# Kernel optimization log

Measured on AMD Instinct MI355X. Metric: run time of the kernel, lower is better.

The kernel has to match this reference:

```python
import jax, jax.numpy as jnp
import numpy as np

EMBED = 1024
HEADS = 16
HD = EMBED // HEADS          # 64
M = 32                       # num_features
R = 2                        # num_quadrature_nodes
EPS = 1e-06
C_CONST = 2.0 + EPS
CHUNK = 512


def setup_inputs() -> dict:
    key = jax.random.key(0)
    ks = jax.random.split(key, 4)
    B, T = 2, 2048
    x = jax.random.normal(ks[0], (B, T, EMBED), jnp.float32)
    Wqkv = jax.random.normal(ks[1], (EMBED, 3 * EMBED), jnp.float32) * 0.02
    bqkv = jnp.zeros((3 * EMBED,), jnp.float32)
    Wout = jax.random.normal(ks[2], (EMBED, EMBED), jnp.float32) * 0.02
    bout = jnp.zeros((EMBED,), jnp.float32)
    omega = jax.random.normal(ks[3], (R, HEADS, HD, M), jnp.float32)
    # Gauss-Laguerre quadrature buffers (deterministic)
    nodes, weights = np.polynomial.laguerre.laggauss(R)
    quad_nodes = jnp.asarray(nodes / C_CONST, jnp.float32)
    quad_weights = jnp.asarray(weights * (C_CONST / 4.0), jnp.float32)
    return {"x": x, "Wqkv": Wqkv, "bqkv": bqkv, "Wout": Wout, "bout": bout,
            "omega": omega, "quad_nodes": quad_nodes, "quad_weights": quad_weights}


def _features(x, omega, quad_nodes, quad_weights):
    # x: (B,H,T,D) -> Laplace PRF features (B,H,T,R*M)
    B, H, T, D = x.shape
    xn = x / jnp.maximum(jnp.linalg.norm(x, axis=-1, keepdims=True), 1e-12)
    proj = jnp.einsum('bhtd,rhdm->rbhtm', xn, omega)
    s = quad_nodes[:, None, None, None, None]
    sqrt_2s = jnp.sqrt(2.0 * jnp.maximum(s, 0.0))
    arg = jnp.clip(proj * sqrt_2s - s, -20.0, 20.0)
    feat = jnp.exp(arg) / np.sqrt(M).astype(np.float32)
    feat = feat * jnp.sqrt(jnp.maximum(quad_weights, 0.0))[:, None, None, None, None]
    return jnp.transpose(feat, (1, 2, 3, 0, 4)).reshape(B, H, T, R * M)


def reference(x, Wqkv, bqkv, Wout, bout, omega, quad_nodes, quad_weights):
    B, T, C = x.shape
    qkv = x @ Wqkv + bqkv
    q, k, v = jnp.split(qkv, 3, axis=-1)
    resh = lambda t: t.reshape(B, T, HEADS, HD).transpose(0, 2, 1, 3)  # (B,H,T,D)
    q, k, v = resh(q), resh(k), resh(v)
    qf = _features(q, omega, quad_nodes, quad_weights)   # (B,H,T,F)
    kf = _features(k, omega, quad_nodes, quad_weights)
    Fd = R * M
    nc = T // CHUNK
    # -> (nc, B, H, chunk, .)
    to_chunks = lambda t, last: t.reshape(B, HEADS, nc, CHUNK, last).transpose(2, 0, 1, 3, 4)
    qc = to_chunks(qf, Fd)
    kc = to_chunks(kf, Fd)
    vc = to_chunks(v, HD)

    def step(carry, inp):
        kv_state, k_state = carry                        # (B,H,F,D), (B,H,F)
        q_ch, k_ch, v_ch = inp
        kv_prod = jnp.einsum('bhtf,bhtd->bhtfd', k_ch, v_ch)
        kv_cur = jnp.cumsum(kv_prod, axis=2) + kv_state[:, :, None]
        k_cur = jnp.cumsum(k_ch, axis=2) + k_state[:, :, None]
        ctx = jnp.einsum('bhtf,bhtfd->bhtd', q_ch, kv_cur)
        den = jnp.maximum(jnp.einsum('bhtf,bhtf->bht', q_ch, k_cur), 1e-06)
        out_ch = ctx / den[..., None]
        return (kv_cur[:, :, -1], k_cur[:, :, -1]), out_ch

    init = (jnp.zeros((B, HEADS, Fd, HD), jnp.float32),
            jnp.zeros((B, HEADS, Fd), jnp.float32))
    _, outs = jax.lax.scan(step, init, (qc, kc, vc))     # (nc,B,H,chunk,D)
    out = outs.transpose(1, 2, 0, 3, 4).reshape(B, HEADS, T, HD)
    out = out.transpose(0, 2, 1, 3).reshape(B, T, C)
    return out @ Wout + bout
```

## Files before the change

kernel.cpp:

```cpp
#include <hip/hip_runtime.h>
#include <cstddef>
#include <cstdint>

#define B_ 2
#define T_ 2048
#define EMBED_ 1024
#define HEADS_ 16
#define HD_ 64
#define M_ 32
#define R_ 2
#define FD_ 64
#define LCH 64
#define NCH (T_ / LCH)
#define BH_ (B_ * HEADS_)

typedef unsigned short u16;
using bf16x8 = __attribute__((ext_vector_type(8))) short;
using f16x8 = __attribute__((ext_vector_type(8))) _Float16;
using f32x4 = __attribute__((ext_vector_type(4))) float;

__device__ __forceinline__ u16 f2bf(float f) {
  uint32_t u = __float_as_uint(f);
  u += 0x7FFF + ((u >> 16) & 1);
  return (u16)(u >> 16);
}
__device__ __forceinline__ float bf2f(u16 h) {
  return __uint_as_float(((uint32_t)h) << 16);
}
__device__ __forceinline__ u16 f2h(float f) {
  _Float16 h = (_Float16)f;
  return *(u16*)&h;
}
__device__ __forceinline__ _Float16 f2hh(float f) { return (_Float16)f; }

__device__ __forceinline__ void gload_lds16(const void* g, void* l) {
  __builtin_amdgcn_global_load_lds(
      (const __attribute__((address_space(1))) unsigned int*)g,
      (__attribute__((address_space(3))) unsigned int*)l, 16, 0, 0);
}

__device__ __forceinline__ int swz_off(int R, int s) {
  return (R >> 1) * 64 + (((((R & 1) << 2) | s) ^ ((R >> 1) & 7)) * 8);
}

__global__ __launch_bounds__(256) void gemm_f16_k(
    const u16* __restrict__ A, const u16* __restrict__ Bt,
    const float* __restrict__ bias, float* __restrict__ C, int K, int ldc)
{
  __shared__ u16 As[2][128 * 32];
  __shared__ u16 Bs[2][128 * 32];
  const int tid = threadIdx.x;
  const int row0 = blockIdx.y * 128, col0 = blockIdx.x * 128;
  const int lane = tid & 63;
  const int w = tid >> 6;
  const int wr = tid >> 7, wc = (tid >> 6) & 1;
  f32x4 acc[4][4];
#pragma unroll
  for (int m = 0; m < 4; ++m)
#pragma unroll
    for (int n = 0; n < 4; ++n)
#pragma unroll
      for (int r = 0; r < 4; ++r) acc[m][n][r] = 0.f;

  const int u_ = (lane & 7) ^ (lane >> 3);
  const int srow = w * 16 + 2 * (lane >> 3) + (u_ >> 2);
  const int skp = (u_ & 3) * 8;
  const u16* Agp = A + (size_t)(row0 + srow) * K + skp;
  const u16* Bgp = Bt + (size_t)(col0 + srow) * K + skp;
  const int wb = w * 512;

  const int fr = lane & 15;
  const int s_ = lane >> 4;
  int aoff[4], boff[4];
#pragma unroll
  for (int m = 0; m < 4; ++m) aoff[m] = swz_off(wr * 64 + m * 16 + fr, s_);
#pragma unroll
  for (int n = 0; n < 4; ++n) boff[n] = swz_off(wc * 64 + n * 16 + fr, s_);

  const int nt = K >> 5;
  gload_lds16(Agp, &As[0][wb]);
  gload_lds16(Agp + (size_t)64 * K, &As[0][wb + 2048]);
  gload_lds16(Bgp, &Bs[0][wb]);
  gload_lds16(Bgp + (size_t)64 * K, &Bs[0][wb + 2048]);
  __syncthreads();

  for (int t = 0; t < nt; ++t) {
    const int cur = t & 1;
    if (t + 1 < nt) {
      const int k0 = (t + 1) * 32;
      gload_lds16(Agp + k0, &As[cur ^ 1][wb]);
      gload_lds16(Agp + k0 + (size_t)64 * K, &As[cur ^ 1][wb + 2048]);
      gload_lds16(Bgp + k0, &Bs[cur ^ 1][wb]);
      gload_lds16(Bgp + k0 + (size_t)64 * K, &Bs[cur ^ 1][wb + 2048]);
    }
    f16x8 a[4], b[4];
#pragma unroll
    for (int m = 0; m < 4; ++m) a[m] = *(const f16x8*)&As[cur][aoff[m]];
#pragma unroll
    for (int n = 0; n < 4; ++n) b[n] = *(const f16x8*)&Bs[cur][boff[n]];
#pragma unroll
    for (int m = 0; m < 4; ++m)
#pragma unroll
      for (int n = 0; n < 4; ++n)
        acc[m][n] = __builtin_amdgcn_mfma_f32_16x16x32_f16(a[m], b[n],
                                                           acc[m][n], 0, 0, 0);
    __syncthreads();
  }
  const int fg = lane >> 4;
#pragma unroll
  for (int m = 0; m < 4; ++m) {
#pragma unroll
    for (int n = 0; n < 4; ++n) {
      const int col = col0 + wc * 64 + n * 16 + fr;
      const float bv = bias[col];
#pragma unroll
      for (int r = 0; r < 4; ++r) {
        const int row = row0 + wr * 64 + m * 16 + fg * 4 + r;
        C[(size_t)row * ldc + col] = acc[m][n][r] + bv;
      }
    }
  }
}

__global__ __launch_bounds__(256) void gemm_f16_n64_k(
    const u16* __restrict__ A, const u16* __restrict__ Bt,
    const float* __restrict__ bias, float* __restrict__ C, int K, int ldc)
{
  __shared__ u16 As[2][128 * 32];
  __shared__ u16 Bs[2][64 * 32];
  const int tid = threadIdx.x;
  const int row0 = blockIdx.y * 128, col0 = blockIdx.x * 64;
  const int lane = tid & 63;
  const int w = tid >> 6;
  f32x4 acc[2][4];
#pragma unroll
  for (int m = 0; m < 2; ++m)
#pragma unroll
    for (int n = 0; n < 4; ++n)
#pragma unroll
      for (int r = 0; r < 4; ++r) acc[m][n][r] = 0.f;

  const int u_ = (lane & 7) ^ (lane >> 3);
  const int srow = w * 16 + 2 * (lane >> 3) + (u_ >> 2);
  const int skp = (u_ & 3) * 8;
  const u16* Agp = A + (size_t)(row0 + srow) * K + skp;
  const u16* Bgp = Bt + (size_t)(col0 + srow) * K + skp;
  const int wb = w * 512;

  const int fr = lane & 15;
  const int s_ = lane >> 4;
  int aoff[2], boff[4];
#pragma unroll
  for (int m = 0; m < 2; ++m) aoff[m] = swz_off(w * 32 + m * 16 + fr, s_);
#pragma unroll
  for (int n = 0; n < 4; ++n) boff[n] = swz_off(n * 16 + fr, s_);

  const int nt = K >> 5;
  gload_lds16(Agp, &As[0][wb]);
  gload_lds16(Agp + (size_t)64 * K, &As[0][wb + 2048]);
  gload_lds16(Bgp, &Bs[0][wb]);
  __syncthreads();

  for (int t = 0; t < nt; ++t) {
    const int cur = t & 1;
    if (t + 1 < nt) {
      const int k0 = (t + 1) * 32;
      gload_lds16(Agp + k0, &As[cur ^ 1][wb]);
      gload_lds16(Agp + k0 + (size_t)64 * K, &As[cur ^ 1][wb + 2048]);
      gload_lds16(Bgp + k0, &Bs[cur ^ 1][wb]);
    }
    f16x8 a[2], b[4];
#pragma unroll
    for (int m = 0; m < 2; ++m) a[m] = *(const f16x8*)&As[cur][aoff[m]];
#pragma unroll
    for (int n = 0; n < 4; ++n) b[n] = *(const f16x8*)&Bs[cur][boff[n]];
#pragma unroll
    for (int m = 0; m < 2; ++m)
#pragma unroll
      for (int n = 0; n < 4; ++n)
        acc[m][n] = __builtin_amdgcn_mfma_f32_16x16x32_f16(a[m], b[n],
                                                           acc[m][n], 0, 0, 0);
    __syncthreads();
  }
  const int fg = lane >> 4;
#pragma unroll
  for (int m = 0; m < 2; ++m) {
#pragma unroll
    for (int n = 0; n < 4; ++n) {
      const int col = col0 + n * 16 + fr;
      const float bv = bias[col];
#pragma unroll
      for (int r = 0; r < 4; ++r) {
        const int row = row0 + w * 32 + m * 16 + fg * 4 + r;
        C[(size_t)row * ldc + col] = acc[m][n][r] + bv;
      }
    }
  }
}

__global__ __launch_bounds__(256) void cvt_x_f16_k(const float* __restrict__ X,
                                                   u16* __restrict__ Y, int n8)
{
  const int idx = blockIdx.x * 256 + threadIdx.x;
  if (idx >= n8) return;
  float4 a = *(const float4*)&X[(size_t)idx * 8];
  float4 b = *(const float4*)&X[(size_t)idx * 8 + 4];
  ushort4 o0, o1;
  o0.x = f2h(a.x); o0.y = f2h(a.y); o0.z = f2h(a.z); o0.w = f2h(a.w);
  o1.x = f2h(b.x); o1.y = f2h(b.y); o1.z = f2h(b.z); o1.w = f2h(b.w);
  *(ushort4*)&Y[(size_t)idx * 8] = o0;
  *(ushort4*)&Y[(size_t)idx * 8 + 4] = o1;
}

__global__ __launch_bounds__(256) void cvt_w_f16t_k(const float* __restrict__ W,
                                                    u16* __restrict__ Wt, int N)
{
  __shared__ float tile[32][33];
  const int n0 = blockIdx.x * 32, k0 = blockIdx.y * 32;
  const int tx = threadIdx.x & 31, ty = threadIdx.x >> 5;
#pragma unroll
  for (int i = 0; i < 4; ++i)
    tile[ty + i * 8][tx] = W[(size_t)(k0 + ty + i * 8) * N + n0 + tx];
  __syncthreads();
#pragma unroll
  for (int i = 0; i < 4; ++i) {
    const int n = ty + i * 8;
    Wt[(size_t)(n0 + n) * 1024 + k0 + tx] = f2h(tile[tx][n]);
  }
}

__global__ __launch_bounds__(256) void gemm_bias_k(
    const float* __restrict__ A, const float* __restrict__ Bm,
    const float* __restrict__ bias, float* __restrict__ C,
    int Mdim, int Ndim, int Kdim, int lda, int ldb, int ldc)
{
  __shared__ float Asm[16][128];
  __shared__ float Bsm[16][128];
  const int tid = threadIdx.x;
  const int row0 = blockIdx.y * 128;
  const int col0 = blockIdx.x * 128;
  const int ty = tid >> 4, tx = tid & 15;
  float acc[8][8];
#pragma unroll
  for (int i = 0; i < 8; ++i)
#pragma unroll
    for (int j = 0; j < 8; ++j) acc[i][j] = 0.f;

  for (int k0 = 0; k0 < Kdim; k0 += 16) {
#pragma unroll
    for (int l = 0; l < 2; ++l) {
      int f = tid * 2 + l;
      int ar = f >> 2, aq = f & 3;
      float4 av = *reinterpret_cast<const float4*>(
          &A[(size_t)(row0 + ar) * lda + k0 + aq * 4]);
      Asm[aq * 4 + 0][ar] = av.x;
      Asm[aq * 4 + 1][ar] = av.y;
      Asm[aq * 4 + 2][ar] = av.z;
      Asm[aq * 4 + 3][ar] = av.w;
      int br = f >> 5, bc = f & 31;
      *reinterpret_cast<float4*>(&Bsm[br][bc * 4]) =
          *reinterpret_cast<const float4*>(
              &Bm[(size_t)(k0 + br) * ldb + col0 + bc * 4]);
    }
    __syncthreads();
#pragma unroll
    for (int kk = 0; kk < 16; ++kk) {
      float a[8], b[8];
      *reinterpret_cast<float4*>(&a[0]) =
          *reinterpret_cast<const float4*>(&Asm[kk][ty * 8]);
      *reinterpret_cast<float4*>(&a[4]) =
          *reinterpret_cast<const float4*>(&Asm[kk][ty * 8 + 4]);
      *reinterpret_cast<float4*>(&b[0]) =
          *reinterpret_cast<const float4*>(&Bsm[kk][tx * 8]);
      *reinterpret_cast<float4*>(&b[4]) =
          *reinterpret_cast<const float4*>(&Bsm[kk][tx * 8 + 4]);
#pragma unroll
      for (int i = 0; i < 8; ++i)
#pragma unroll
        for (int j = 0; j < 8; ++j) acc[i][j] += a[i] * b[j];
    }
    __syncthreads();
  }
#pragma unroll
  for (int i = 0; i < 8; ++i) {
    int r = row0 + ty * 8 + i;
#pragma unroll
    for (int j = 0; j < 8; j += 4) {
      int c = col0 + tx * 8 + j;
      float4 o;
      o.x = acc[i][j + 0] + bias[c + 0];
      o.y = acc[i][j + 1] + bias[c + 1];
      o.z = acc[i][j + 2] + bias[c + 2];
      o.w = acc[i][j + 3] + bias[c + 3];
      *reinterpret_cast<float4*>(&C[(size_t)r * ldc + c]) = o;
    }
  }
}

__global__ __launch_bounds__(256) void features_mfma_k(
    const float* __restrict__ qkv, const float* __restrict__ omega,
    const float* __restrict__ qnodes, const float* __restrict__ qweights,
    float* __restrict__ qf, float* __restrict__ kf)
{
  __shared__ u16 Aext[64 * 200];
  __shared__ u16 Bext[64 * 200];
  __shared__ float rinv_s[64];
  const int tid = threadIdx.x;
  const int t0 = blockIdx.x * 64;
  const int h = blockIdx.y;
  const int b = blockIdx.z & 1;
  const int which = blockIdx.z >> 1;
  const int bh = b * HEADS_ + h;

  {
    const int row = tid >> 2;
    const int seg = (tid & 3) * 16;
    const float* xsrc = &qkv[((size_t)(b * T_ + t0 + row)) * 3072 +
                             which * 1024 + h * 64 + seg];
    float xv[16];
#pragma unroll
    for (int q = 0; q < 4; ++q)
      *(float4*)&xv[q * 4] = *(const float4*)&xsrc[q * 4];
    float ss = 0.f;
#pragma unroll
    for (int j = 0; j < 16; ++j) ss += xv[j] * xv[j];
    ss += __shfl_xor(ss, 1, 64);
    ss += __shfl_xor(ss, 2, 64);
    if ((tid & 3) == 0) rinv_s[row] = 1.f / fmaxf(sqrtf(ss), 1e-12f);
    ushort4 hv[4], lv[4];
    u16* hp = (u16*)hv; u16* lp = (u16*)lv;
#pragma unroll
    for (int j = 0; j < 16; ++j) {
      u16 hh = f2bf(xv[j]);
      hp[j] = hh;
      lp[j] = f2bf(xv[j] - bf2f(hh));
    }
    u16* arow = &Aext[row * 200 + seg];
#pragma unroll
    for (int q = 0; q < 4; ++q) {
      *(ushort4*)&arow[q * 4] = hv[q];
      *(ushort4*)&arow[64 + q * 4] = lv[q];
      *(ushort4*)&arow[128 + q * 4] = hv[q];
    }
  }
  {
    const int r_o = tid >> 7;
    const int dseg = (tid >> 5) & 3;
    const int m_o = tid & 31;
    const int n = r_o * 32 + m_o;
    const size_t obase =
        (((size_t)(r_o * HEADS_ + h)) * HD_ + dseg * 16) * M_ + m_o;
    ushort4 hv[4], lv[4];
    u16* hp = (u16*)hv; u16* lp = (u16*)lv;
#pragma unroll
    for (int i = 0; i < 16; ++i) {
      float v = omega[obase + (size_t)i * M_];
      u16 hh = f2bf(v);
      hp[i] = hh;
      lp[i] = f2bf(v - bf2f(hh));
    }
    u16* brow = &Bext[n * 200 + dseg * 16];
#pragma unroll
    for (int q = 0; q < 4; ++q) {
      *(ushort4*)&brow[q * 4] = hv[q];
      *(ushort4*)&brow[64 + q * 4] = hv[q];
      *(ushort4*)&brow[128 + q * 4] = lv[q];
    }
  }
  __syncthreads();

  const int lane = tid & 63;
  const int w = tid >> 6;
  const int fr = lane & 15, s_ = lane >> 4;
  f32x4 facc[4];
#pragma unroll
  for (int n = 0; n < 4; ++n)
#pragma unroll
    for (int r = 0; r < 4; ++r) facc[n][r] = 0.f;
  const u16* arow = &Aext[(w * 16 + fr) * 200 + s_ * 8];
#pragma unroll
  for (int kk = 0; kk < 6; ++kk) {
    bf16x8 av = *(const bf16x8*)&arow[kk * 32];
#pragma unroll
    for (int n = 0; n < 4; ++n) {
      bf16x8 bv = *(const bf16x8*)&Bext[(n * 16 + fr) * 200 + kk * 32 + s_ * 8];
      facc[n] = __builtin_amdgcn_mfma_f32_16x16x32_bf16(av, bv, facc[n], 0, 0, 0);
    }
  }

  const float s0 = qnodes[0], s1 = qnodes[1];
  const float sq0 = sqrtf(2.f * fmaxf(s0, 0.f));
  const float sq1 = sqrtf(2.f * fmaxf(s1, 0.f));
  const float sc0 = sqrtf(fmaxf(qweights[0], 0.f)) * 0.17677669529663687f;
  const float sc1 = sqrtf(fmaxf(qweights[1], 0.f)) * 0.17677669529663687f;
  float* __restrict__ dst = which ? kf : qf;
  const size_t base = ((size_t)bh * T_ + t0) * FD_;
  const int fg = lane >> 4;
#pragma unroll
  for (int n = 0; n < 4; ++n) {
    const int feat = n * 16 + fr;
    const int ridx = n >> 1;
    const float sq = ridx ? sq1 : sq0;
    const float so = ridx ? s1 : s0;
    const float sc = ridx ? sc1 : sc0;
#pragma unroll
    for (int j = 0; j < 4; ++j) {
      const int token = w * 16 + fg * 4 + j;
      const float pr = facc[n][j] * rinv_s[token];
      float arg = fminf(fmaxf(pr * sq - so, -20.f), 20.f);
      dst[base + (size_t)token * FD_ + feat] = expf(arg) * sc;
    }
  }
}

__global__ __launch_bounds__(256) void chunk_sums_k(
    const float* __restrict__ kf, const float* __restrict__ qkv,
    float* __restrict__ kvsum, float* __restrict__ ksum)
{
  const int blk = blockIdx.x;
  const int c = blk % NCH;
  const int bh = blk / NCH;
  const int b = bh / HEADS_, h = bh % HEADS_;
  const int tid = threadIdx.x;
  const int d = tid & 63;
  const int fq = tid >> 6;
  __shared__ float kf_s[16][64];
  __shared__ float v_s[16][64];
  float acc[16];
#pragma unroll
  for (int i = 0; i < 16; ++i) acc[i] = 0.f;
  float ks = 0.f;
  for (int t0 = 0; t0 < LCH; t0 += 16) {
#pragma unroll
    for (int l = 0; l < 4; ++l) {
      int idx = tid + l * 256;
      int rr = idx >> 6, cc = idx & 63;
      int t = c * LCH + t0 + rr;
      kf_s[rr][cc] = kf[((size_t)bh * T_ + t) * FD_ + cc];
      v_s[rr][cc] =
          qkv[((size_t)(b * T_ + t)) * 3072 + 2 * EMBED_ + h * HD_ + cc];
    }
    __syncthreads();
#pragma unroll
    for (int tt = 0; tt < 16; ++tt) {
      float vv = v_s[tt][d];
      if (fq == 0) ks += kf_s[tt][d];
#pragma unroll
      for (int i = 0; i < 16; ++i) acc[i] += kf_s[tt][fq * 16 + i] * vv;
    }
    __syncthreads();
  }
#pragma unroll
  for (int i = 0; i < 16; ++i)
    kvsum[(size_t)blk * 4096 + (size_t)(fq * 16 + i) * 64 + d] = acc[i];
  if (fq == 0) ksum[(size_t)blk * 64 + d] = ks;
}

__global__ __launch_bounds__(256) void prefix2_k(float* __restrict__ kvsum,
                                                 float* __restrict__ ksum)
{
  const int bh = blockIdx.x >> 4;
  const int eb = blockIdx.x & 15;
  const int e = eb * 256 + threadIdx.x;
  float v[NCH];
  const size_t base = (size_t)bh * NCH * 4096 + e;
#pragma unroll
  for (int c = 0; c < NCH; ++c) v[c] = kvsum[base + (size_t)c * 4096];
  float run = 0.f;
#pragma unroll
  for (int c = 0; c < NCH; ++c) {
    kvsum[base + (size_t)c * 4096] = run;
    run += v[c];
  }
  if (eb == 0 && threadIdx.x < 64) {
    const size_t kb = (size_t)bh * NCH * 64 + threadIdx.x;
    float w[NCH];
#pragma unroll
    for (int c = 0; c < NCH; ++c) w[c] = ksum[kb + c * 64];
    float r2 = 0.f;
#pragma unroll
    for (int c = 0; c < NCH; ++c) {
      ksum[kb + c * 64] = r2;
      r2 += w[c];
    }
  }
}

__global__ __launch_bounds__(256) void chunk_attn4_k(
    const float* __restrict__ qf, const float* __restrict__ kf,
    const float* __restrict__ qkv_v, const float* __restrict__ kvsum,
    const float* __restrict__ ksum, u16* __restrict__ out_f16)
{
  constexpr float SCL = 1.f / 1024.f;
  constexpr float DEN_EPS = 1e-6f / 1024.f;
  __shared__ u16 qf_h[64 * 72];
  __shared__ u16 kf_h[64 * 72];
  __shared__ u16 st_h[64 * 72];
  __shared__ u16 vt_h[64 * 72];
  __shared__ u16 p_h[64 * 72];
  __shared__ float den_s[64];
  const int blk = blockIdx.x;
  const int c = blk & (NCH - 1);
  const int bh = blk / NCH;
  const int b = bh / HEADS_, h = bh % HEADS_;
  const int tid = threadIdx.x;

  {
    const int r = tid >> 2, q4 = (tid & 3) * 16;
    const size_t fbase = ((size_t)bh * T_ + c * LCH + r) * FD_ + q4;
    const size_t vbase =
        ((size_t)(b * T_ + c * LCH + r)) * 3072 + 2 * EMBED_ + h * HD_ + q4;
    const size_t sbase = (size_t)blk * 4096 + (size_t)r * 64 + q4;
    float qv[16], kv[16], sv[16], vv[16], ks[16];
#pragma unroll
    for (int j = 0; j < 16; j += 4) {
      *(float4*)&qv[j] = *(const float4*)&qf[fbase + j];
      *(float4*)&kv[j] = *(const float4*)&kf[fbase + j];
      *(float4*)&sv[j] = *(const float4*)&kvsum[sbase + j];
      *(float4*)&vv[j] = *(const float4*)&qkv_v[vbase + j];
      *(float4*)&ks[j] = *(const float4*)&ksum[(size_t)blk * 64 + q4 + j];
    }
    float dh = 0.f;
#pragma unroll
    for (int j = 0; j < 16; ++j) dh += qv[j] * ks[j];
    dh += __shfl_xor(dh, 1, 64);
    dh += __shfl_xor(dh, 2, 64);
    if ((tid & 3) == 0) den_s[r] = dh * SCL;
    ushort4 qo[4], ko[4];
    u16* qp = (u16*)qo; u16* kp = (u16*)ko;
#pragma unroll
    for (int j = 0; j < 16; ++j) { qp[j] = f2h(qv[j]); kp[j] = f2h(kv[j]); }
#pragma unroll
    for (int q = 0; q < 4; ++q) {
      *(ushort4*)&qf_h[r * 72 + q4 + q * 4] = qo[q];
      *(ushort4*)&kf_h[r * 72 + q4 + q * 4] = ko[q];
    }
#pragma unroll
    for (int j = 0; j < 16; ++j) {
      st_h[(q4 + j) * 72 + r] = f2h(sv[j] * SCL);
      vt_h[(q4 + j) * 72 + r] = f2h(vv[j]);
    }
  }
  __syncthreads();

  const int lane = tid & 63;
  const int w = tid >> 6;
  const int fr = lane & 15;
  const int s_ = lane >> 4;
  const int arow = (w * 16 + fr) * 72 + s_ * 8;
  const int trow = w * 16 + s_ * 4;

  const f16x8 a0 = *(const f16x8*)&qf_h[arow];
  const f16x8 a1 = *(const f16x8*)&qf_h[arow + 32];

  f32x4 sc[4];
#pragma unroll
  for (int n = 0; n < 4; ++n) {
#pragma unroll
    for (int r = 0; r < 4; ++r) sc[n][r] = 0.f;
    const f16x8 b0 = *(const f16x8*)&kf_h[(n * 16 + fr) * 72 + s_ * 8];
    const f16x8 b1 = *(const f16x8*)&kf_h[(n * 16 + fr) * 72 + 32 + s_ * 8];
    sc[n] = __builtin_amdgcn_mfma_f32_16x16x32_f16(a0, b0, sc[n], 0, 0, 0);
    sc[n] = __builtin_amdgcn_mfma_f32_16x16x32_f16(a1, b1, sc[n], 0, 0, 0);
  }
  f32x4 acc[4];
#pragma unroll
  for (int n = 0; n < 4; ++n) {
#pragma unroll
    for (int r = 0; r < 4; ++r) acc[n][r] = 0.f;
    const f16x8 b0 = *(const f16x8*)&st_h[(n * 16 + fr) * 72 + s_ * 8];
    const f16x8 b1 = *(const f16x8*)&st_h[(n * 16 + fr) * 72 + 32 + s_ * 8];
    acc[n] = __builtin_amdgcn_mfma_f32_16x16x32_f16(a0, b0, acc[n], 0, 0, 0);
    acc[n] = __builtin_amdgcn_mfma_f32_16x16x32_f16(a1, b1, acc[n], 0, 0, 0);
  }
  float den2[4] = {0.f, 0.f, 0.f, 0.f};
#pragma unroll
  for (int n = 0; n < 4; ++n) {
    const int scol = n * 16 + fr;
#pragma unroll
    for (int r = 0; r < 4; ++r) {
      const int t = trow + r;
      const float v = (scol <= t) ? sc[n][r] : 0.f;
      p_h[t * 72 + scol] = f2h(v * SCL);
      den2[r] += v;
    }
  }
#pragma unroll
  for (int r = 0; r < 4; ++r) {
    float d = den2[r];
    d += __shfl_xor(d, 1, 64);
    d += __shfl_xor(d, 2, 64);
    d += __shfl_xor(d, 4, 64);
    d += __shfl_xor(d, 8, 64);
    den2[r] = d;
  }
  if (fr == 0) {
#pragma unroll
    for (int r = 0; r < 4; ++r) den_s[trow + r] += den2[r] * SCL;
  }
  __syncthreads();

  const f16x8 p0 = *(const f16x8*)&p_h[arow];
  const f16x8 p1 = *(const f16x8*)&p_h[arow + 32];
#pragma unroll
  for (int n = 0; n < 4; ++n) {
    const f16x8 b0 = *(const f16x8*)&vt_h[(n * 16 + fr) * 72 + s_ * 8];
    const f16x8 b1 = *(const f16x8*)&vt_h[(n * 16 + fr) * 72 + 32 + s_ * 8];
    acc[n] = __builtin_amdgcn_mfma_f32_16x16x32_f16(p0, b0, acc[n], 0, 0, 0);
    acc[n] = __builtin_amdgcn_mfma_f32_16x16x32_f16(p1, b1, acc[n], 0, 0, 0);
  }

  float rden[4];
#pragma unroll
  for (int r = 0; r < 4; ++r)
    rden[r] = 1.f / fmaxf(den_s[trow + r], DEN_EPS);
#pragma unroll
  for (int n = 0; n < 4; ++n) {
    const int d = n * 16 + fr;
#pragma unroll
    for (int r = 0; r < 4; ++r) {
      const int t = trow + r;
      out_f16[((size_t)(b * T_ + c * LCH + t)) * 1024 + h * HD_ + d] =
          f2h(acc[n][r] * rden[r]);
    }
  }
}

__global__ __launch_bounds__(256) void chunk_attn3_k(
    const float* __restrict__ qf, const float* __restrict__ kf,
    const float* __restrict__ qkv_v, const float* __restrict__ kvsum,
    const float* __restrict__ ksum, float* __restrict__ out_f32, int lda)
{
  const int blk = blockIdx.x;
  const int c = blk & (NCH - 1);
  const int bh = blk / NCH;
  const int b = bh / HEADS_, h = bh % HEADS_;
  const int tid = threadIdx.x;
  __shared__ float kf_s[64][64];
  __shared__ float v_s[64][64];
  __shared__ float S_s[64][64];
  __shared__ float qf_s[64][64];
  {
    const int r = tid >> 2, q4 = (tid & 3) * 16;
    const size_t fbase = ((size_t)bh * T_ + c * LCH + r) * FD_ + q4;
    const size_t vbase =
        ((size_t)(b * T_ + c * LCH + r)) * 3072 + 2 * EMBED_ + h * HD_ + q4;
    const size_t sbase = (size_t)blk * 4096 + (size_t)r * 64 + q4;
#pragma unroll
    for (int j = 0; j < 16; j += 4) {
      *(float4*)&kf_s[r][q4 + j] = *(const float4*)&kf[fbase + j];
      *(float4*)&qf_s[r][q4 + j] = *(const float4*)&qf[fbase + j];
      *(float4*)&S_s[r][q4 + j] = *(const float4*)&kvsum[sbase + j];
      *(float4*)&v_s[r][q4 + j] = *(const float4*)&qkv_v[vbase + j];
    }
  }
  __syncthreads();
  const int l = tid & 63;
  const int t = (tid >> 6) * 16 + (l & 15);
  const int dq = l >> 4, d0 = dq * 16;

  float q_r[64];
#pragma unroll
  for (int j = 0; j < 64; j += 4)
    *(float4*)&q_r[j] = *(const float4*)&qf_s[t][j];

  float ctx[16];
#pragma unroll
  for (int j = 0; j < 16; ++j) ctx[j] = 0.f;
  float den = 0.f, den2 = 0.f;

#pragma unroll 4
  for (int f = 0; f < 64; ++f) {
    const float qv = q_r[f];
#pragma unroll
    for (int j = 0; j < 16; j += 4) {
      float4 s4 = *(const float4*)&S_s[f][d0 + j];
      ctx[j + 0] += qv * s4.x;
      ctx[j + 1] += qv * s4.y;
      ctx[j + 2] += qv * s4.z;
      ctx[j + 3] += qv * s4.w;
    }
  }
  {
    const float* svp = &ksum[(size_t)blk * 64 + d0];
#pragma unroll
    for (int j = 0; j < 16; ++j) den += q_r[d0 + j] * svp[j];
  }

  for (int s = 0; s < LCH; ++s) {
    float a = 0.f;
#pragma unroll
    for (int j = 0; j < 16; j += 4) {
      float4 k4 = *(const float4*)&kf_s[s][d0 + j];
      a += q_r[d0 + j] * k4.x + q_r[d0 + j + 1] * k4.y +
           q_r[d0 + j + 2] * k4.z + q_r[d0 + j + 3] * k4.w;
    }
    a += __shfl_xor(a, 16, 64);
    a += __shfl_xor(a, 32, 64);
    if (s <= t) {
      den2 += a;
#pragma unroll
      for (int j = 0; j < 16; j += 4) {
        float4 v4 = *(const float4*)&v_s[s][d0 + j];
        ctx[j + 0] += a * v4.x;
        ctx[j + 1] += a * v4.y;
        ctx[j + 2] += a * v4.z;
        ctx[j + 3] += a * v4.w;
      }
    }
  }
  den += __shfl_xor(den, 16, 64);
  den += __shfl_xor(den, 32, 64);
  const float rden = 1.f / fmaxf(den + den2, 1e-6f);
  float* op = &out_f32[((size_t)(b * T_ + c * LCH + t)) * lda + h * HD_ + d0];
#pragma unroll
  for (int j = 0; j < 16; j += 4) {
    float4 o;
    o.x = ctx[j + 0] * rden;
    o.y = ctx[j + 1] * rden;
    o.z = ctx[j + 2] * rden;
    o.w = ctx[j + 3] * rden;
    *(float4*)&op[j] = o;
  }
}

extern "C" void kernel_launch(void* const* d_in, const int* in_sizes, int n_in,
                              void* d_out, int out_size, void* d_ws,
                              size_t ws_size, hipStream_t stream)
{
  (void)in_sizes; (void)n_in; (void)out_size;
  const float* x = (const float*)d_in[0];
  const float* Wqkv = (const float*)d_in[1];
  const float* bqkv = (const float*)d_in[2];
  const float* Wout = (const float*)d_in[3];
  const float* bout = (const float*)d_in[4];
  const float* omega = (const float*)d_in[5];
  const float* qnodes = (const float*)d_in[6];
  const float* qweights = (const float*)d_in[7];
  float* out = (float*)d_out;

  float* ws = (float*)d_ws;
  const size_t QKV_F = (size_t)B_ * T_ * 3 * EMBED_;
  const size_t F_F = (size_t)BH_ * T_ * FD_;
  const size_t KV_F = (size_t)BH_ * NCH * FD_ * HD_;
  const size_t KS_F = (size_t)BH_ * NCH * FD_;
  const size_t XH_E = (size_t)B_ * T_ * EMBED_;
  const size_t WQ_E = (size_t)3 * EMBED_ * EMBED_;
  const size_t WO_E = (size_t)EMBED_ * EMBED_;

  float* qkv = ws;
  float* qf = qkv + QKV_F;
  float* kf = qf + F_F;
  float* kvsum = kf + F_F;
  float* ksum = kvsum + KV_F;
  u16* x_f16 = (u16*)(ksum + KS_F);
  u16* wq_f16t = x_f16 + XH_E;
  u16* wo_f16t = wq_f16t + WQ_E;
  const size_t needed =
      (QKV_F + 2 * F_F + KV_F + KS_F) * 4 + (XH_E + WQ_E + WO_E) * 2;

  const int MT = B_ * T_;

  if (ws_size >= needed) {
    u16* attn_f16 = x_f16;

    cvt_x_f16_k<<<dim3(2048), 256, 0, stream>>>(x, x_f16, MT * EMBED_ / 8);
    cvt_w_f16t_k<<<dim3(96, 32), 256, 0, stream>>>(Wqkv, wq_f16t, 3 * EMBED_);
    gemm_f16_k<<<dim3(24, 32), 256, 0, stream>>>(x_f16, wq_f16t, bqkv, qkv,
                                                 1024, 3 * EMBED_);
    features_mfma_k<<<dim3(T_ / 64, HEADS_, 4), 256, 0, stream>>>(
        qkv, omega, qnodes, qweights, qf, kf);
    chunk_sums_k<<<dim3(BH_ * NCH), 256, 0, stream>>>(kf, qkv, kvsum, ksum);
    prefix2_k<<<dim3(512), 256, 0, stream>>>(kvsum, ksum);
    cvt_w_f16t_k<<<dim3(32, 32), 256, 0, stream>>>(Wout, wo_f16t, EMBED_);
    chunk_attn4_k<<<dim3(BH_ * NCH), 256, 0, stream>>>(qf, kf, qkv, kvsum,
                                                       ksum, attn_f16);
    gemm_f16_n64_k<<<dim3(16, 32), 256, 0, stream>>>(attn_f16, wo_f16t, bout,
                                                     out, 1024, EMBED_);
  } else {
    gemm_bias_k<<<dim3(24, 32), 256, 0, stream>>>(
        x, Wqkv, bqkv, qkv, MT, 3 * EMBED_, EMBED_, EMBED_, 3 * EMBED_,
        3 * EMBED_);
    features_mfma_k<<<dim3(T_ / 64, HEADS_, 4), 256, 0, stream>>>(
        qkv, omega, qnodes, qweights, qf, kf);
    chunk_sums_k<<<dim3(BH_ * NCH), 256, 0, stream>>>(kf, qkv, kvsum, ksum);
    prefix2_k<<<dim3(512), 256, 0, stream>>>(kvsum, ksum);
    chunk_attn3_k<<<dim3(BH_ * NCH), 256, 0, stream>>>(
        qf, kf, qkv, kvsum, ksum, qkv, 3 * EMBED_);
    gemm_bias_k<<<dim3(8, 32), 256, 0, stream>>>(
        qkv, Wout, bout, out, MT, EMBED_, EMBED_, 3 * EMBED_, EMBED_, EMBED_);
  }
}
```

Baseline: 221.0 us.

## Store features and V in fp16 head-major layout; MFMA chunk sums

The features kernel now writes q/k features as fp16 instead of fp32. The QKV GEMM epilogue writes the V slice directly as fp16 in a (B,H,T,D) layout rather than fp32 into the interleaved qkv buffer. A new chunk_sums_f16_k computes per-chunk K^T V with MFMA from the fp16 tensors, and chunk_attn4_k reads fp16 inputs, skipping its own conversion. This halves intermediate memory traffic and removes scalar reductions, at the cost of fp16 rounding in the chunk-sum accumulation inputs and a scattered epilogue store for V.

```diff
diff --git a/kernel.cpp b/kernel.cpp
--- a/kernel.cpp
+++ b/kernel.cpp
@@ -31,7 +31,9 @@
   _Float16 h = (_Float16)f;
   return *(u16*)&h;
 }
-__device__ __forceinline__ _Float16 f2hh(float f) { return (_Float16)f; }
+__device__ __forceinline__ float h2f(u16 h) {
+  return (float)(*(const _Float16*)&h);
+}
 
 __device__ __forceinline__ void gload_lds16(const void* g, void* l) {
   __builtin_amdgcn_global_load_lds(
@@ -45,7 +47,8 @@
 
 __global__ __launch_bounds__(256) void gemm_f16_k(
     const u16* __restrict__ A, const u16* __restrict__ Bt,
-    const float* __restrict__ bias, float* __restrict__ C, int K, int ldc)
+    const float* __restrict__ bias, float* __restrict__ C, int K, int ldc,
+    u16* __restrict__ V16)
 {
   __shared__ u16 As[2][128 * 32];
   __shared__ u16 Bs[2][128 * 32];
@@ -116,7 +119,14 @@
 #pragma unroll
       for (int r = 0; r < 4; ++r) {
         const int row = row0 + wr * 64 + m * 16 + fg * 4 + r;
-        C[(size_t)row * ldc + col] = acc[m][n][r] + bv;
+        const float val = acc[m][n][r] + bv;
+        if (V16 && col >= 2048) {
+          const int bb = row >> 11, tt = row & 2047;
+          const int hh = (col - 2048) >> 6, dd = col & 63;
+          V16[(((size_t)bb * HEADS_ + hh) * T_ + tt) * 64 + dd] = f2h(val);
+        } else {
+          C[(size_t)row * ldc + col] = val;
+        }
       }
     }
   }
@@ -300,7 +310,7 @@
 __global__ __launch_bounds__(256) void features_mfma_k(
     const float* __restrict__ qkv, const float* __restrict__ omega,
     const float* __restrict__ qnodes, const float* __restrict__ qweights,
-    float* __restrict__ qf, float* __restrict__ kf)
+    void* __restrict__ qfv, void* __restrict__ kfv, int f16out)
 {
   __shared__ u16 Aext[64 * 200];
   __shared__ u16 Bext[64 * 200];
@@ -393,7 +403,7 @@
   const float sq1 = sqrtf(2.f * fmaxf(s1, 0.f));
   const float sc0 = sqrtf(fmaxf(qweights[0], 0.f)) * 0.17677669529663687f;
   const float sc1 = sqrtf(fmaxf(qweights[1], 0.f)) * 0.17677669529663687f;
-  float* __restrict__ dst = which ? kf : qf;
+  void* dstv = which ? kfv : qfv;
   const size_t base = ((size_t)bh * T_ + t0) * FD_;
   const int fg = lane >> 4;
 #pragma unroll
@@ -408,7 +418,76 @@
       const int token = w * 16 + fg * 4 + j;
       const float pr = facc[n][j] * rinv_s[token];
       float arg = fminf(fmaxf(pr * sq - so, -20.f), 20.f);
-      dst[base + (size_t)token * FD_ + feat] = expf(arg) * sc;
+      const float val = expf(arg) * sc;
+      if (f16out)
+        ((u16*)dstv)[base + (size_t)token * FD_ + feat] = f2h(val);
+      else
+        ((float*)dstv)[base + (size_t)token * FD_ + feat] = val;
+    }
+  }
+}
+
+__global__ __launch_bounds__(256) void chunk_sums_f16_k(
+    const u16* __restrict__ kf16, const u16* __restrict__ v16,
+    float* __restrict__ kvsum, float* __restrict__ ksum)
+{
+  __shared__ u16 kfT[64 * 72];
+  __shared__ u16 vT[64 * 72];
+  const int blk = blockIdx.x;
+  const int c = blk & (NCH - 1);
+  const int bh = blk / NCH;
+  const int tid = threadIdx.x;
+  {
+    const int r = tid >> 2, q4 = (tid & 3) * 16;
+    const u16* kp = &kf16[((size_t)bh * T_ + c * LCH + r) * 64 + q4];
+    const u16* vp = &v16[((size_t)bh * T_ + c * LCH + r) * 64 + q4];
+    u16 kv[16], vv[16];
+    *(uint4*)&kv[0] = *(const uint4*)&kp[0];
+    *(uint4*)&kv[8] = *(const uint4*)&kp[8];
+    *(uint4*)&vv[0] = *(const uint4*)&vp[0];
+    *(uint4*)&vv[8] = *(const uint4*)&vp[8];
+#pragma unroll
+    for (int j = 0; j < 16; ++j) {
+      kfT[(q4 + j) * 72 + r] = kv[j];
+      vT[(q4 + j) * 72 + r] = vv[j];
+    }
+  }
+  __syncthreads();
+
+  if (tid < 64) {
+    const _Float16* rp = (const _Float16*)&kfT[tid * 72];
+    float s = 0.f;
+#pragma unroll
+    for (int i = 0; i < 8; ++i) {
+      f16x8 vv = *(const f16x8*)&rp[i * 8];
+#pragma unroll
+      for (int j = 0; j < 8; ++j) s += (float)vv[j];
+    }
+    ksum[(size_t)blk * 64 + tid] = s;
+  }
+
+  const int lane = tid & 63;
+  const int w = tid >> 6;
+  const int fr = lane & 15, s_ = lane >> 4;
+  const f16x8 a0 = *(const f16x8*)&kfT[(w * 16 + fr) * 72 + s_ * 8];
+  const f16x8 a1 = *(const f16x8*)&kfT[(w * 16 + fr) * 72 + 32 + s_ * 8];
+  f32x4 acc[4];
+#pragma unroll
+  for (int n = 0; n < 4; ++n) {
+#pragma unroll
+    for (int r = 0; r < 4; ++r) acc[n][r] = 0.f;
+    const f16x8 b0 = *(const f16x8*)&vT[(n * 16 + fr) * 72 + s_ * 8];
+    const f16x8 b1 = *(const f16x8*)&vT[(n * 16 + fr) * 72 + 32 + s_ * 8];
+    acc[n] = __builtin_amdgcn_mfma_f32_16x16x32_f16(a0, b0, acc[n], 0, 0, 0);
+    acc[n] = __builtin_amdgcn_mfma_f32_16x16x32_f16(a1, b1, acc[n], 0, 0, 0);
+  }
+#pragma unroll
+  for (int n = 0; n < 4; ++n) {
+    const int d = n * 16 + fr;
+#pragma unroll
+    for (int r = 0; r < 4; ++r) {
+      const int f = w * 16 + s_ * 4 + r;
+      kvsum[(size_t)blk * 4096 + (size_t)f * 64 + d] = acc[n][r];
     }
   }
 }
@@ -487,8 +566,8 @@
 }
 
 __global__ __launch_bounds__(256) void chunk_attn4_k(
-    const float* __restrict__ qf, const float* __restrict__ kf,
-    const float* __restrict__ qkv_v, const float* __restrict__ kvsum,
+    const u16* __restrict__ qf16, const u16* __restrict__ kf16,
+    const u16* __restrict__ v16, const float* __restrict__ kvsum,
     const float* __restrict__ ksum, u16* __restrict__ out_f16)
 {
   constexpr float SCL = 1.f / 1024.f;
@@ -507,38 +586,35 @@
 
   {
     const int r = tid >> 2, q4 = (tid & 3) * 16;
-    const size_t fbase = ((size_t)bh * T_ + c * LCH + r) * FD_ + q4;
-    const size_t vbase =
-        ((size_t)(b * T_ + c * LCH + r)) * 3072 + 2 * EMBED_ + h * HD_ + q4;
+    const size_t fbase = ((size_t)bh * T_ + c * LCH + r) * 64 + q4;
     const size_t sbase = (size_t)blk * 4096 + (size_t)r * 64 + q4;
-    float qv[16], kv[16], sv[16], vv[16], ks[16];
+    u16 qv[16], kv[16], vv[16];
+    *(uint4*)&qv[0] = *(const uint4*)&qf16[fbase];
+    *(uint4*)&qv[8] = *(const uint4*)&qf16[fbase + 8];
+    *(uint4*)&kv[0] = *(const uint4*)&kf16[fbase];
+    *(uint4*)&kv[8] = *(const uint4*)&kf16[fbase + 8];
+    *(uint4*)&vv[0] = *(const uint4*)&v16[fbase];
+    *(uint4*)&vv[8] = *(const uint4*)&v16[fbase + 8];
+    float sv[16], ks[16];
 #pragma unroll
     for (int j = 0; j < 16; j += 4) {
-      *(float4*)&qv[j] = *(const float4*)&qf[fbase + j];
-      *(float4*)&kv[j] = *(const float4*)&kf[fbase + j];
       *(float4*)&sv[j] = *(const float4*)&kvsum[sbase + j];
-      *(float4*)&vv[j] = *(const float4*)&qkv_v[vbase + j];
       *(float4*)&ks[j] = *(const float4*)&ksum[(size_t)blk * 64 + q4 + j];
     }
     float dh = 0.f;
 #pragma unroll
-    for (int j = 0; j < 16; ++j) dh += qv[j] * ks[j];
+    for (int j = 0; j < 16; ++j) dh += h2f(qv[j]) * ks[j];
     dh += __shfl_xor(dh, 1, 64);
     dh += __shfl_xor(dh, 2, 64);
     if ((tid & 3) == 0) den_s[r] = dh * SCL;
-    ushort4 qo[4], ko[4];
-    u16* qp = (u16*)qo; u16* kp = (u16*)ko;
-#pragma unroll
-    for (int j = 0; j < 16; ++j) { qp[j] = f2h(qv[j]); kp[j] = f2h(kv[j]); }
-#pragma unroll
-    for (int q = 0; q < 4; ++q) {
-      *(ushort4*)&qf_h[r * 72 + q4 + q * 4] = qo[q];
-      *(ushort4*)&kf_h[r * 72 + q4 + q * 4] = ko[q];
-    }
+    *(uint4*)&qf_h[r * 72 + q4] = *(const uint4*)&qv[0];
+    *(uint4*)&qf_h[r * 72 + q4 + 8] = *(const uint4*)&qv[8];
+    *(uint4*)&kf_h[r * 72 + q4] = *(const uint4*)&kv[0];
+    *(uint4*)&kf_h[r * 72 + q4 + 8] = *(const uint4*)&kv[8];
 #pragma unroll
     for (int j = 0; j < 16; ++j) {
       st_h[(q4 + j) * 72 + r] = f2h(sv[j] * SCL);
-      vt_h[(q4 + j) * 72 + r] = f2h(vv[j]);
+      vt_h[(q4 + j) * 72 + r] = vv[j];
     }
   }
   __syncthreads();
@@ -748,18 +824,19 @@
   const size_t WQ_E = (size_t)3 * EMBED_ * EMBED_;
   const size_t WO_E = (size_t)EMBED_ * EMBED_;
 
+  const int MT = B_ * T_;
+
   float* qkv = ws;
-  float* qf = qkv + QKV_F;
-  float* kf = qf + F_F;
-  float* kvsum = kf + F_F;
+  u16* qf16 = (u16*)(qkv + QKV_F);
+  u16* kf16 = qf16 + F_F;
+  u16* v16 = kf16 + F_F;
+  float* kvsum = (float*)(v16 + F_F);
   float* ksum = kvsum + KV_F;
   u16* x_f16 = (u16*)(ksum + KS_F);
   u16* wq_f16t = x_f16 + XH_E;
   u16* wo_f16t = wq_f16t + WQ_E;
-  const size_t needed =
-      (QKV_F + 2 * F_F + KV_F + KS_F) * 4 + (XH_E + WQ_E + WO_E) * 2;
-
-  const int MT = B_ * T_;
+  const size_t needed = QKV_F * 4 + 3 * F_F * 2 + (KV_F + KS_F) * 4 +
+                        (XH_E + WQ_E + WO_E) * 2;
 
   if (ws_size >= needed) {
     u16* attn_f16 = x_f16;
@@ -767,26 +844,31 @@
     cvt_x_f16_k<<<dim3(2048), 256, 0, stream>>>(x, x_f16, MT * EMBED_ / 8);
     cvt_w_f16t_k<<<dim3(96, 32), 256, 0, stream>>>(Wqkv, wq_f16t, 3 * EMBED_);
     gemm_f16_k<<<dim3(24, 32), 256, 0, stream>>>(x_f16, wq_f16t, bqkv, qkv,
-                                                 1024, 3 * EMBED_);
+                                                 1024, 3 * EMBED_, v16);
     features_mfma_k<<<dim3(T_ / 64, HEADS_, 4), 256, 0, stream>>>(
-        qkv, omega, qnodes, qweights, qf, kf);
-    chunk_sums_k<<<dim3(BH_ * NCH), 256, 0, stream>>>(kf, qkv, kvsum, ksum);
+        qkv, omega, qnodes, qweights, qf16, kf16, 1);
+    chunk_sums_f16_k<<<dim3(BH_ * NCH), 256, 0, stream>>>(kf16, v16, kvsum,
+                                                          ksum);
     prefix2_k<<<dim3(512), 256, 0, stream>>>(kvsum, ksum);
     cvt_w_f16t_k<<<dim3(32, 32), 256, 0, stream>>>(Wout, wo_f16t, EMBED_);
-    chunk_attn4_k<<<dim3(BH_ * NCH), 256, 0, stream>>>(qf, kf, qkv, kvsum,
+    chunk_attn4_k<<<dim3(BH_ * NCH), 256, 0, stream>>>(qf16, kf16, v16, kvsum,
                                                        ksum, attn_f16);
     gemm_f16_n64_k<<<dim3(16, 32), 256, 0, stream>>>(attn_f16, wo_f16t, bout,
                                                      out, 1024, EMBED_);
   } else {
+    float* qf = qkv + QKV_F;
+    float* kf = qf + F_F;
+    float* kvs = kf + F_F;
+    float* kss = kvs + KV_F;
     gemm_bias_k<<<dim3(24, 32), 256, 0, stream>>>(
         x, Wqkv, bqkv, qkv, MT, 3 * EMBED_, EMBED_, EMBED_, 3 * EMBED_,
         3 * EMBED_);
     features_mfma_k<<<dim3(T_ / 64, HEADS_, 4), 256, 0, stream>>>(
-        qkv, omega, qnodes, qweights, qf, kf);
-    chunk_sums_k<<<dim3(BH_ * NCH), 256, 0, stream>>>(kf, qkv, kvsum, ksum);
-    prefix2_k<<<dim3(512), 256, 0, stream>>>(kvsum, ksum);
+        qkv, omega, qnodes, qweights, qf, kf, 0);
+    chunk_sums_k<<<dim3(BH_ * NCH), 256, 0, stream>>>(kf, qkv, kvs, kss);
+    prefix2_k<<<dim3(512), 256, 0, stream>>>(kvs, kss);
     chunk_attn3_k<<<dim3(BH_ * NCH), 256, 0, stream>>>(
-        qf, kf, qkv, kvsum, ksum, qkv, 3 * EMBED_);
+        qf, kf, qkv, kvs, kss, qkv, 3 * EMBED_);
     gemm_bias_k<<<dim3(8, 32), 256, 0, stream>>>(
         qkv, Wout, bout, out, MT, EMBED_, EMBED_, 3 * EMBED_, EMBED_, EMBED_);
   }
```

Result: faster. 193.3 us (-12.6%).
